# Kernel optimization log

Hardware: AMD Instinct MI355X
Metric: run time of the kernel (lower is better)

The kernel has to match this reference:

```python
import jax, jax.numpy as jnp
import numpy as np

N_NODES = 100000
IN_DIM = 128
HIDDEN = 256
N_EDGES = 1600000


def gcn_conv(x, W, b, src, dst, n_nodes):
    """PyG GCNConv: add self-loops, symmetric deg^-1/2 normalization, linear, aggregate."""
    h = x @ W  # [N, out]
    # degrees with self-loops (edge weight 1 each)
    deg = jax.ops.segment_sum(jnp.ones_like(dst, dtype=h.dtype), dst, num_segments=n_nodes)
    dinv = jax.lax.rsqrt(jnp.maximum(deg, 1e-12))
    norm = dinv[src] * dinv[dst]  # [E+N]
    msg = h[src] * norm[:, None]  # [E+N, out]
    out = jax.ops.segment_sum(msg, dst, num_segments=n_nodes)
    return out + b


def setup_inputs() -> dict:
    key = jax.random.key(0)
    k1, k2, k3, k4 = jax.random.split(key, 4)
    x = jax.random.normal(k1, (N_NODES, IN_DIM), dtype=jnp.float32)
    edge_index = jax.random.randint(k2, (2, N_EDGES), 0, N_NODES, dtype=jnp.int64)
    # Glorot-style init for weights, zero bias (as in PyG GCNConv defaults)
    W1 = jax.random.normal(k3, (IN_DIM, HIDDEN), dtype=jnp.float32) / np.sqrt(IN_DIM)
    b1 = jnp.zeros((HIDDEN,), dtype=jnp.float32)
    W2 = jax.random.normal(k4, (HIDDEN, 1), dtype=jnp.float32) / np.sqrt(HIDDEN)
    b2 = jnp.zeros((1,), dtype=jnp.float32)
    return {"x": x, "edge_index": edge_index, "W1": W1, "b1": b1, "W2": W2, "b2": b2}


def reference(x, edge_index, W1, b1, W2, b2):
    n = x.shape[0]
    loops = jnp.arange(n, dtype=edge_index.dtype)
    src = jnp.concatenate([edge_index[0], loops])
    dst = jnp.concatenate([edge_index[1], loops])
    h = gcn_conv(x, W1, b1, src, dst, n)
    h = jax.nn.relu(h)
    # dropout p=0.5 is identity in eval mode (training=False)
    out = gcn_conv(h, W2, b2, src, dst, n)
    return out
```

## Files before the change

### kernel.cpp

```cpp
#include <hip/hip_runtime.h>
#include <hip/hip_bf16.h>


typedef __attribute__((ext_vector_type(8))) short bf16x8;
typedef __attribute__((ext_vector_type(4))) float f32x4;

#define SLOTS 48

__device__ __forceinline__ unsigned short f2bf(float f) {
  unsigned int x = __builtin_bit_cast(unsigned int, f);
  unsigned int r = x + 0x7FFFu + ((x >> 16) & 1u);
  return (unsigned short)(r >> 16);
}
__device__ __forceinline__ float bf2f(unsigned short h) {
  unsigned int x = ((unsigned int)h) << 16;
  return __builtin_bit_cast(float, x);
}

__device__ __forceinline__ long long ld_idx(const void* ei, long long i, int is64) {
  if (is64) return ((const long long*)ei)[i];
  return (long long)((const int*)ei)[i];
}

__global__ void k_detect(const void* __restrict__ ei, int E, int N, int* __restrict__ flag) {
  __shared__ int bad;
  if (threadIdx.x == 0) bad = 0;
  __syncthreads();
  int cnt = min(E, 1024);
  int lb = 0;
  for (int i = threadIdx.x; i < cnt; i += blockDim.x) {
    long long v = ((const long long*)ei)[i];
    if (v < 0 || v >= (long long)N) lb = 1;
  }
  if (lb) atomicOr(&bad, 1);
  __syncthreads();
  if (threadIdx.x == 0) *flag = bad ? 0 : 1;
}

__global__ void k_zero_i32(int* __restrict__ p, int n) {
  int i = blockIdx.x * blockDim.x + threadIdx.x;
  if (i < n) p[i] = 0;
}

__global__ void k_xq(const float4* __restrict__ X4, int4* __restrict__ Xq, int total8) {
  int i = blockIdx.x * blockDim.x + threadIdx.x;
  if (i >= total8) return;
  float4 u = X4[i * 2], v = X4[i * 2 + 1];
  int q0 = max(-32767, min(32767, __float2int_rn(u.x * 4096.f)));
  int q1 = max(-32767, min(32767, __float2int_rn(u.y * 4096.f)));
  int q2 = max(-32767, min(32767, __float2int_rn(u.z * 4096.f)));
  int q3 = max(-32767, min(32767, __float2int_rn(u.w * 4096.f)));
  int q4 = max(-32767, min(32767, __float2int_rn(v.x * 4096.f)));
  int q5 = max(-32767, min(32767, __float2int_rn(v.y * 4096.f)));
  int q6 = max(-32767, min(32767, __float2int_rn(v.z * 4096.f)));
  int q7 = max(-32767, min(32767, __float2int_rn(v.w * 4096.f)));
  int4 o;
  o.x = (q0 & 0xFFFF) | (q1 << 16);
  o.y = (q2 & 0xFFFF) | (q3 << 16);
  o.z = (q4 & 0xFFFF) | (q5 << 16);
  o.w = (q6 & 0xFFFF) | (q7 << 16);
  Xq[i] = o;
}

__global__ void k_deg(const void* __restrict__ ei, int E, const int* __restrict__ flag,
                      int* __restrict__ deg, int* __restrict__ bucket) {
  int e = blockIdx.x * blockDim.x + threadIdx.x;
  if (e >= E) return;
  int is64 = *flag;
  int s = (int)ld_idx(ei, e, is64);
  int d = (int)ld_idx(ei, (long long)E + e, is64);
  int slot = atomicAdd(&deg[d], 1);
  if (slot < SLOTS) bucket[(size_t)d * SLOTS + slot] = s;
}

__device__ __forceinline__ void acc_i16x8(const int4 v, const float w, float* a) {
  a[0] += w * (float)(short)(v.x);
  a[1] += w * (float)(v.x >> 16);
  a[2] += w * (float)(short)(v.y);
  a[3] += w * (float)(v.y >> 16);
  a[4] += w * (float)(short)(v.z);
  a[5] += w * (float)(v.z >> 16);
  a[6] += w * (float)(short)(v.w);
  a[7] += w * (float)(v.w >> 16);
}

__global__ __launch_bounds__(256) void k_gather(
    const short* __restrict__ Xq, const float4* __restrict__ Xf4,
    const int* __restrict__ bucket, const int* __restrict__ deg,
    unsigned short* __restrict__ Ahi, unsigned short* __restrict__ Alo, int N) {
  int g = blockIdx.x * 16 + (threadIdx.x >> 4);
  int gl = threadIdx.x & 15;
  if (g >= N) return;
  int l8 = gl * 8;
  int dg = deg[g];
  float di = rsqrtf((float)(dg + 1));
  const int* bsrc = bucket + (size_t)g * SLOTS;
  int n = min(dg, SLOTS);
  float a[8] = {0.f, 0.f, 0.f, 0.f, 0.f, 0.f, 0.f, 0.f};
  int e = 0;
  for (; e + 8 <= n; e += 8) {
    int s[8];
    int4 xv[8];
    float w[8];
    #pragma unroll
    for (int u = 0; u < 8; ++u) s[u] = bsrc[e + u];
    #pragma unroll
    for (int u = 0; u < 8; ++u)
      xv[u] = *(const int4*)(Xq + (size_t)s[u] * 128 + l8);
    #pragma unroll
    for (int u = 0; u < 8; ++u) w[u] = rsqrtf((float)(deg[s[u]] + 1));
    #pragma unroll
    for (int u = 0; u < 8; ++u) acc_i16x8(xv[u], w[u], a);
  }
  for (; e < n; ++e) {
    int s = bsrc[e];
    int4 xv = *(const int4*)(Xq + (size_t)s * 128 + l8);
    acc_i16x8(xv, rsqrtf((float)(deg[s] + 1)), a);
  }
  const float S = 1.0f / 4096.0f;
  float4 xa = Xf4[(size_t)g * 32 + gl * 2];
  float4 xb = Xf4[(size_t)g * 32 + gl * 2 + 1];
  a[0] = di * (a[0] * S + di * xa.x);
  a[1] = di * (a[1] * S + di * xa.y);
  a[2] = di * (a[2] * S + di * xa.z);
  a[3] = di * (a[3] * S + di * xa.w);
  a[4] = di * (a[4] * S + di * xb.x);
  a[5] = di * (a[5] * S + di * xb.y);
  a[6] = di * (a[6] * S + di * xb.z);
  a[7] = di * (a[7] * S + di * xb.w);
  unsigned short h[8];
  int4 hv, lv;
  #pragma unroll
  for (int j = 0; j < 8; ++j) h[j] = f2bf(a[j]);
  hv.x = (unsigned)h[0] | ((unsigned)h[1] << 16);
  hv.y = (unsigned)h[2] | ((unsigned)h[3] << 16);
  hv.z = (unsigned)h[4] | ((unsigned)h[5] << 16);
  hv.w = (unsigned)h[6] | ((unsigned)h[7] << 16);
  unsigned short l[8];
  #pragma unroll
  for (int j = 0; j < 8; ++j) l[j] = f2bf(a[j] - bf2f(h[j]));
  lv.x = (unsigned)l[0] | ((unsigned)l[1] << 16);
  lv.y = (unsigned)l[2] | ((unsigned)l[3] << 16);
  lv.z = (unsigned)l[4] | ((unsigned)l[5] << 16);
  lv.w = (unsigned)l[6] | ((unsigned)l[7] << 16);
  *(int4*)(Ahi + (size_t)g * 128 + l8) = hv;
  *(int4*)(Alo + (size_t)g * 128 + l8) = lv;
}

__global__ void k_w1prep(const float* __restrict__ W1, int4* __restrict__ Bpk) {
  int tid = blockIdx.x * 256 + threadIdx.x;
  int lane = tid & 63, ks = (tid >> 6) & 3, ct = tid >> 8;
  int c = ct >> 2, fi = (ct & 3) * 4 + ks;
  int kbase = ks * 32 + (lane >> 4) * 8;
  int col = ct * 16 + (lane & 15);
  unsigned short h[8], lo[8];
  #pragma unroll
  for (int j = 0; j < 8; ++j) {
    float w = W1[(size_t)(kbase + j) * 256 + col];
    h[j] = f2bf(w);
    lo[j] = f2bf(w - bf2f(h[j]));
  }
  int4 hv, lv;
  hv.x = (unsigned)h[0] | ((unsigned)h[1] << 16);
  hv.y = (unsigned)h[2] | ((unsigned)h[3] << 16);
  hv.z = (unsigned)h[4] | ((unsigned)h[5] << 16);
  hv.w = (unsigned)h[6] | ((unsigned)h[7] << 16);
  lv.x = (unsigned)lo[0] | ((unsigned)lo[1] << 16);
  lv.y = (unsigned)lo[2] | ((unsigned)lo[3] << 16);
  lv.z = (unsigned)lo[4] | ((unsigned)lo[5] << 16);
  lv.w = (unsigned)lo[6] | ((unsigned)lo[7] << 16);
  Bpk[c * 2048 + fi * 64 + lane] = hv;
  Bpk[c * 2048 + 1024 + fi * 64 + lane] = lv;
}

__global__ __launch_bounds__(256) void k_gemm_mfma(
    const unsigned short* __restrict__ Ahi, const unsigned short* __restrict__ Alo,
    const int4* __restrict__ Bpk, const float* __restrict__ b1,
    const float* __restrict__ W2, float* __restrict__ z, int N) {
  __shared__ int4 lb[2][2048];
  int tid = threadIdx.x;
  int wv = tid >> 6, lane = tid & 63;
  int m0 = (blockIdx.x * 4 + wv) * 32;
  if (m0 > N - 32) m0 = N - 32;
  int cl = lane & 15, g = lane >> 4;

  for (int i = tid; i < 2048; i += 256) lb[0][i] = Bpk[i];

  const bf16x8* arh0 = (const bf16x8*)(Ahi + (size_t)(m0 + cl) * 128 + g * 8);
  const bf16x8* arl0 = (const bf16x8*)(Alo + (size_t)(m0 + cl) * 128 + g * 8);
  const bf16x8* arh1 = (const bf16x8*)(Ahi + (size_t)(m0 + 16 + cl) * 128 + g * 8);
  const bf16x8* arl1 = (const bf16x8*)(Alo + (size_t)(m0 + 16 + cl) * 128 + g * 8);
  bf16x8 ah0[4], al0[4], ah1[4], al1[4];
  #pragma unroll
  for (int ks = 0; ks < 4; ++ks) {
    ah0[ks] = arh0[ks * 4];
    al0[ks] = arl0[ks * 4];
    ah1[ks] = arh1[ks * 4];
    al1[ks] = arl1[ks * 4];
  }

  f32x4 acc0[16], acc1[16];
  #pragma unroll
  for (int ct = 0; ct < 16; ++ct) {
    acc0[ct] = (f32x4){0.f, 0.f, 0.f, 0.f};
    acc1[ct] = (f32x4){0.f, 0.f, 0.f, 0.f};
  }

  #pragma unroll
  for (int c = 0; c < 4; ++c) {
    __syncthreads();
    if (c < 3) {
      for (int i = tid; i < 2048; i += 256) lb[(c + 1) & 1][i] = Bpk[(c + 1) * 2048 + i];
    }
    const int4* lbuf = lb[c & 1];
    #pragma unroll
    for (int ks = 0; ks < 4; ++ks) {
      #pragma unroll
      for (int i = 0; i < 4; ++i) {
        int ct = c * 4 + i;
        int fi = i * 4 + ks;
        bf16x8 bh = __builtin_bit_cast(bf16x8, lbuf[fi * 64 + lane]);
        bf16x8 bl = __builtin_bit_cast(bf16x8, lbuf[1024 + fi * 64 + lane]);
        acc0[ct] = __builtin_amdgcn_mfma_f32_16x16x32_bf16(ah0[ks], bh, acc0[ct], 0, 0, 0);
        acc0[ct] = __builtin_amdgcn_mfma_f32_16x16x32_bf16(ah0[ks], bl, acc0[ct], 0, 0, 0);
        acc0[ct] = __builtin_amdgcn_mfma_f32_16x16x32_bf16(al0[ks], bh, acc0[ct], 0, 0, 0);
        acc1[ct] = __builtin_amdgcn_mfma_f32_16x16x32_bf16(ah1[ks], bh, acc1[ct], 0, 0, 0);
        acc1[ct] = __builtin_amdgcn_mfma_f32_16x16x32_bf16(ah1[ks], bl, acc1[ct], 0, 0, 0);
        acc1[ct] = __builtin_amdgcn_mfma_f32_16x16x32_bf16(al1[ks], bh, acc1[ct], 0, 0, 0);
      }
    }
  }

  float p0 = 0.f, p1 = 0.f, p2 = 0.f, p3 = 0.f;
  float q0 = 0.f, q1 = 0.f, q2 = 0.f, q3 = 0.f;
  #pragma unroll
  for (int ct = 0; ct < 16; ++ct) {
    float bb = b1[ct * 16 + cl];
    float ww = W2[ct * 16 + cl];
    p0 += fmaxf(acc0[ct][0] + bb, 0.f) * ww;
    p1 += fmaxf(acc0[ct][1] + bb, 0.f) * ww;
    p2 += fmaxf(acc0[ct][2] + bb, 0.f) * ww;
    p3 += fmaxf(acc0[ct][3] + bb, 0.f) * ww;
    q0 += fmaxf(acc1[ct][0] + bb, 0.f) * ww;
    q1 += fmaxf(acc1[ct][1] + bb, 0.f) * ww;
    q2 += fmaxf(acc1[ct][2] + bb, 0.f) * ww;
    q3 += fmaxf(acc1[ct][3] + bb, 0.f) * ww;
  }
  #pragma unroll
  for (int s = 1; s < 16; s <<= 1) {
    p0 += __shfl_xor(p0, s); p1 += __shfl_xor(p1, s);
    p2 += __shfl_xor(p2, s); p3 += __shfl_xor(p3, s);
    q0 += __shfl_xor(q0, s); q1 += __shfl_xor(q1, s);
    q2 += __shfl_xor(q2, s); q3 += __shfl_xor(q3, s);
  }
  float pv = (cl == 0) ? p0 : (cl == 1) ? p1 : (cl == 2) ? p2 : p3;
  float qv = (cl == 0) ? q0 : (cl == 1) ? q1 : (cl == 2) ? q2 : q3;
  if (cl < 4) {
    z[m0 + 4 * g + cl] = pv;
    z[m0 + 16 + 4 * g + cl] = qv;
  }
}

__global__ void k_outgather(const int* __restrict__ bucket, const int* __restrict__ deg,
                            const float* __restrict__ z, const float* __restrict__ b2,
                            float* __restrict__ out, int N) {
  int i = blockIdx.x * blockDim.x + threadIdx.x;
  if (i >= N) return;
  int dg = deg[i];
  float di = rsqrtf((float)(dg + 1));
  float acc = di * z[i];
  const int* bsrc = bucket + (size_t)i * SLOTS;
  int n = min(dg, SLOTS);
  for (int e = 0; e < n; ++e) {
    int s = bsrc[e];
    acc += rsqrtf((float)(deg[s] + 1)) * z[s];
  }
  out[i] = di * acc + b2[0];
}

extern "C" void kernel_launch(void* const* d_in, const int* in_sizes, int n_in,
                              void* d_out, int out_size, void* d_ws, size_t ws_size,
                              hipStream_t stream) {
  const float* x  = (const float*)d_in[0];
  const void*  ei = d_in[1];
  const float* W1 = (const float*)d_in[2];
  const float* b1 = (const float*)d_in[3];
  const float* W2 = (const float*)d_in[4];
  const float* b2 = (const float*)d_in[5];
  float* out = (float*)d_out;

  int N = in_sizes[0] / 128;
  int E = in_sizes[1] / 2;

  char* ws = (char*)d_ws;
  size_t o = 0;
  unsigned short* Ahi = (unsigned short*)(ws + o); o += (size_t)N * 128 * 2;
  unsigned short* Alo = (unsigned short*)(ws + o); o += (size_t)N * 128 * 2;
  short* Xq = (short*)(ws + o); o += (size_t)N * 128 * 2;
  int* bucket = (int*)(ws + o); o += (size_t)N * SLOTS * 4;
  o = (o + 255) & ~(size_t)255;
  int* deg = (int*)(ws + o); o += (size_t)N * 4;
  int* flag = (int*)(ws + o); o += 4;
  o = (o + 255) & ~(size_t)255;
  float* z = (float*)(ws + o); o += (size_t)N * 4;
  o = (o + 255) & ~(size_t)255;
  int4* Bpk = (int4*)(ws + o); o += 131072;

  k_detect<<<1, 256, 0, stream>>>(ei, E, N, flag);
  k_zero_i32<<<(N + 255) / 256, 256, 0, stream>>>(deg, N);
  k_xq<<<(N * 16 + 255) / 256, 256, 0, stream>>>((const float4*)x, (int4*)Xq, N * 16);
  k_w1prep<<<16, 256, 0, stream>>>(W1, Bpk);
  k_deg<<<(E + 255) / 256, 256, 0, stream>>>(ei, E, flag, deg, bucket);
  k_gather<<<(N + 15) / 16, 256, 0, stream>>>(Xq, (const float4*)x, bucket, deg,
                                              Ahi, Alo, N);
  k_gemm_mfma<<<(N + 127) / 128, 256, 0, stream>>>(Ahi, Alo, Bpk, b1, W2, z, N);
  k_outgather<<<(N + 255) / 256, 256, 0, stream>>>(bucket, deg, z, b2, out, N);
}
```

Baseline: 362.8 us.

## Partition degree scatter by destination range and prescale layer-2 values

The degree/bucket build now uses a grid-stride loop where each block handles only destinations in one of eight node ranges. The goal is better locality for the atomics and bucket writes, at the cost of reading the destination index array eight times. The self-loop term in the first gather now reads the quantized features instead of the fp32 input, which trades some precision for less traffic. The GEMM epilogue pre-multiplies z by deg^-1/2, so the output gather sums prescaled values with four accumulators instead of loading per-neighbor degrees.

```diff
diff --git a/kernel.cpp b/kernel.cpp
--- a/kernel.cpp
+++ b/kernel.cpp
@@ -6,6 +6,7 @@
 typedef __attribute__((ext_vector_type(4))) float f32x4;
 
 #define SLOTS 48
+#define NPART 8
 
 __device__ __forceinline__ unsigned short f2bf(float f) {
   unsigned int x = __builtin_bit_cast(unsigned int, f);
@@ -62,15 +63,23 @@
   Xq[i] = o;
 }
 
-__global__ void k_deg(const void* __restrict__ ei, int E, const int* __restrict__ flag,
-                      int* __restrict__ deg, int* __restrict__ bucket) {
-  int e = blockIdx.x * blockDim.x + threadIdx.x;
-  if (e >= E) return;
+__global__ void k_deg(const void* __restrict__ ei, int E, int N,
+                      const int* __restrict__ flag, int* __restrict__ deg,
+                      int* __restrict__ bucket) {
+  int p = blockIdx.x & (NPART - 1);
+  int r = blockIdx.x >> 3;
+  int R = gridDim.x >> 3;
+  int np = (N + NPART - 1) / NPART;
+  int lo = p * np, hi = min(N, lo + np);
   int is64 = *flag;
-  int s = (int)ld_idx(ei, e, is64);
-  int d = (int)ld_idx(ei, (long long)E + e, is64);
-  int slot = atomicAdd(&deg[d], 1);
-  if (slot < SLOTS) bucket[(size_t)d * SLOTS + slot] = s;
+  int stride = R * blockDim.x;
+  for (int e = r * blockDim.x + threadIdx.x; e < E; e += stride) {
+    int d = (int)ld_idx(ei, (long long)E + e, is64);
+    if (d < lo || d >= hi) continue;
+    int s = (int)ld_idx(ei, e, is64);
+    int slot = atomicAdd(&deg[d], 1);
+    if (slot < SLOTS) bucket[(size_t)d * SLOTS + slot] = s;
+  }
 }
 
 __device__ __forceinline__ void acc_i16x8(const int4 v, const float w, float* a) {
@@ -85,9 +94,9 @@
 }
 
 __global__ __launch_bounds__(256) void k_gather(
-    const short* __restrict__ Xq, const float4* __restrict__ Xf4,
-    const int* __restrict__ bucket, const int* __restrict__ deg,
-    unsigned short* __restrict__ Ahi, unsigned short* __restrict__ Alo, int N) {
+    const short* __restrict__ Xq, const int* __restrict__ bucket,
+    const int* __restrict__ deg, unsigned short* __restrict__ Ahi,
+    unsigned short* __restrict__ Alo, int N) {
   int g = blockIdx.x * 16 + (threadIdx.x >> 4);
   int gl = threadIdx.x & 15;
   if (g >= N) return;
@@ -117,28 +126,21 @@
     int4 xv = *(const int4*)(Xq + (size_t)s * 128 + l8);
     acc_i16x8(xv, rsqrtf((float)(deg[s] + 1)), a);
   }
+  int4 xs = *(const int4*)(Xq + (size_t)g * 128 + l8);
+  acc_i16x8(xs, di, a);
   const float S = 1.0f / 4096.0f;
-  float4 xa = Xf4[(size_t)g * 32 + gl * 2];
-  float4 xb = Xf4[(size_t)g * 32 + gl * 2 + 1];
-  a[0] = di * (a[0] * S + di * xa.x);
-  a[1] = di * (a[1] * S + di * xa.y);
-  a[2] = di * (a[2] * S + di * xa.z);
-  a[3] = di * (a[3] * S + di * xa.w);
-  a[4] = di * (a[4] * S + di * xb.x);
-  a[5] = di * (a[5] * S + di * xb.y);
-  a[6] = di * (a[6] * S + di * xb.z);
-  a[7] = di * (a[7] * S + di * xb.w);
-  unsigned short h[8];
+  #pragma unroll
+  for (int j = 0; j < 8; ++j) a[j] = di * S * a[j];
+  unsigned short h[8], l[8];
+  #pragma unroll
+  for (int j = 0; j < 8; ++j) h[j] = f2bf(a[j]);
+  #pragma unroll
+  for (int j = 0; j < 8; ++j) l[j] = f2bf(a[j] - bf2f(h[j]));
   int4 hv, lv;
-  #pragma unroll
-  for (int j = 0; j < 8; ++j) h[j] = f2bf(a[j]);
   hv.x = (unsigned)h[0] | ((unsigned)h[1] << 16);
   hv.y = (unsigned)h[2] | ((unsigned)h[3] << 16);
   hv.z = (unsigned)h[4] | ((unsigned)h[5] << 16);
   hv.w = (unsigned)h[6] | ((unsigned)h[7] << 16);
-  unsigned short l[8];
-  #pragma unroll
-  for (int j = 0; j < 8; ++j) l[j] = f2bf(a[j] - bf2f(h[j]));
   lv.x = (unsigned)l[0] | ((unsigned)l[1] << 16);
   lv.y = (unsigned)l[2] | ((unsigned)l[3] << 16);
   lv.z = (unsigned)l[4] | ((unsigned)l[5] << 16);
@@ -176,7 +178,8 @@
 __global__ __launch_bounds__(256) void k_gemm_mfma(
     const unsigned short* __restrict__ Ahi, const unsigned short* __restrict__ Alo,
     const int4* __restrict__ Bpk, const float* __restrict__ b1,
-    const float* __restrict__ W2, float* __restrict__ z, int N) {
+    const float* __restrict__ W2, const int* __restrict__ deg,
+    float* __restrict__ zs, int N) {
   __shared__ int4 lb[2][2048];
   int tid = threadIdx.x;
   int wv = tid >> 6, lane = tid & 63;
@@ -256,25 +259,30 @@
   float pv = (cl == 0) ? p0 : (cl == 1) ? p1 : (cl == 2) ? p2 : p3;
   float qv = (cl == 0) ? q0 : (cl == 1) ? q1 : (cl == 2) ? q2 : q3;
   if (cl < 4) {
-    z[m0 + 4 * g + cl] = pv;
-    z[m0 + 16 + 4 * g + cl] = qv;
+    int n0 = m0 + 4 * g + cl, n1 = n0 + 16;
+    zs[n0] = rsqrtf((float)(deg[n0] + 1)) * pv;
+    zs[n1] = rsqrtf((float)(deg[n1] + 1)) * qv;
   }
 }
 
 __global__ void k_outgather(const int* __restrict__ bucket, const int* __restrict__ deg,
-                            const float* __restrict__ z, const float* __restrict__ b2,
+                            const float* __restrict__ zs, const float* __restrict__ b2,
                             float* __restrict__ out, int N) {
   int i = blockIdx.x * blockDim.x + threadIdx.x;
   if (i >= N) return;
   int dg = deg[i];
   float di = rsqrtf((float)(dg + 1));
-  float acc = di * z[i];
+  float acc = zs[i];
   const int* bsrc = bucket + (size_t)i * SLOTS;
   int n = min(dg, SLOTS);
-  for (int e = 0; e < n; ++e) {
-    int s = bsrc[e];
-    acc += rsqrtf((float)(deg[s] + 1)) * z[s];
-  }
+  int e = 0;
+  float a0 = 0.f, a1 = 0.f, a2 = 0.f, a3 = 0.f;
+  for (; e + 4 <= n; e += 4) {
+    int s0 = bsrc[e], s1 = bsrc[e + 1], s2 = bsrc[e + 2], s3 = bsrc[e + 3];
+    a0 += zs[s0]; a1 += zs[s1]; a2 += zs[s2]; a3 += zs[s3];
+  }
+  for (; e < n; ++e) a0 += zs[bsrc[e]];
+  acc += (a0 + a1) + (a2 + a3);
   out[i] = di * acc + b2[0];
 }
 
@@ -302,7 +310,7 @@
   int* deg = (int*)(ws + o); o += (size_t)N * 4;
   int* flag = (int*)(ws + o); o += 4;
   o = (o + 255) & ~(size_t)255;
-  float* z = (float*)(ws + o); o += (size_t)N * 4;
+  float* zs = (float*)(ws + o); o += (size_t)N * 4;
   o = (o + 255) & ~(size_t)255;
   int4* Bpk = (int4*)(ws + o); o += 131072;
 
@@ -310,9 +318,8 @@
   k_zero_i32<<<(N + 255) / 256, 256, 0, stream>>>(deg, N);
   k_xq<<<(N * 16 + 255) / 256, 256, 0, stream>>>((const float4*)x, (int4*)Xq, N * 16);
   k_w1prep<<<16, 256, 0, stream>>>(W1, Bpk);
-  k_deg<<<(E + 255) / 256, 256, 0, stream>>>(ei, E, flag, deg, bucket);
-  k_gather<<<(N + 15) / 16, 256, 0, stream>>>(Xq, (const float4*)x, bucket, deg,
-                                              Ahi, Alo, N);
-  k_gemm_mfma<<<(N + 127) / 128, 256, 0, stream>>>(Ahi, Alo, Bpk, b1, W2, z, N);
-  k_outgather<<<(N + 255) / 256, 256, 0, stream>>>(bucket, deg, z, b2, out, N);
-}
+  k_deg<<<2048, 256, 0, stream>>>(ei, E, N, flag, deg, bucket);
+  k_gather<<<(N + 15) / 16, 256, 0, stream>>>(Xq, bucket, deg, Ahi, Alo, N);
+  k_gemm_mfma<<<(N + 127) / 128, 256, 0, stream>>>(Ahi, Alo, Bpk, b1, W2, deg, zs, N);
+  k_outgather<<<(N + 255) / 256, 256, 0, stream>>>(bucket, deg, zs, b2, out, N);
+}
```

Measured after the change: 297.4 us. 18.0% less time.
